# Kernel tuning notes

Measured on AMD Instinct MI355X. Metric: run time of the kernel, lower is better.

## Reference

```python
import jax, jax.numpy as jnp
import numpy as np

MUL = 32
HEAD_DIM = 16
CLIP = 5.0
EPS = 1e-6
INV_SQRTD = 1.0 / np.sqrt(HEAD_DIM)
ENV_BLOCKS = (1, 3)          # 0e, 1o
TP_BLOCKS = (1, 1, 3, 3)     # 0e(0x0), 0e(1x1), 1o(0x1), 1o(1x0)


def so3_layernorm(x, g, block_dims):
    """x: [..., MUL, D]; per-irrep-block RMS norm over (mul, components), affine scale g [MUL, n_blocks]."""
    out, i = [], 0
    for b, d in enumerate(block_dims):
        blk = x[..., i:i + d]
        n = jnp.sqrt(jnp.mean(blk * blk, axis=(-2, -1), keepdims=True) + EPS)
        out.append(blk / n * g[:, b][:, None])
        i += d
    return jnp.concatenate(out, axis=-1)


def scatter_softmax(logits, seg, num_segments):
    """softmax over edges grouped by destination node. logits [E, M]."""
    m = jax.ops.segment_max(logits, seg, num_segments=num_segments)
    e = jnp.exp(logits - m[seg])
    d = jax.ops.segment_sum(e, seg, num_segments=num_segments)
    return e / d[seg]


def setup_inputs() -> dict:
    key = jax.random.key(0)
    ks = jax.random.split(key, 16)
    N, E, LAT, NODE_DIM, COND, HID = 16384, 262144, 64, 64, 32, 128
    sc = lambda f: f ** -0.5
    return {
        "node_attrs": jax.random.normal(ks[0], (N, NODE_DIM), jnp.float32),
        "scalar_state": jax.random.normal(ks[1], (E, LAT), jnp.float32),
        "equiv_state": jax.random.normal(ks[2], (E, MUL, 4), jnp.float32),
        "edge_conditioning": jax.random.normal(ks[3], (E, COND), jnp.float32),
        "residual_update_coeff": jax.random.uniform(ks[4], (1,), jnp.float32),
        "W_env1": jax.random.normal(ks[5], (LAT + COND, HID), jnp.float32) * sc(LAT + COND),
        "b_env1": jnp.zeros((HID,), jnp.float32),
        "W_env2": jax.random.normal(ks[6], (HID, MUL * 2), jnp.float32) * sc(HID),
        "Wq": jax.random.normal(ks[7], (NODE_DIM, MUL * HEAD_DIM), jnp.float32) * sc(NODE_DIM),
        "Wk": jax.random.normal(ks[8], (LAT, MUL * HEAD_DIM), jnp.float32) * sc(LAT),
        "g_env": jnp.ones((MUL, 2), jnp.float32),
        "g_tp": jnp.ones((MUL, 4), jnp.float32),
        "Wp1": jax.random.normal(ks[9], (MUL * 2 + COND, HID), jnp.float32) * sc(MUL * 2 + COND),
        "bp1": jnp.zeros((HID,), jnp.float32),
        "Wp2": jax.random.normal(ks[10], (HID, LAT + MUL * 4), jnp.float32) * sc(HID),
        "edge_src": jax.random.randint(ks[11], (E,), 0, N),
    }


def reference(node_attrs, scalar_state, equiv_state, edge_conditioning,
              residual_update_coeff, W_env1, b_env1, W_env2, Wq, Wk,
              g_env, g_tp, Wp1, bp1, Wp2, edge_src):
    N = node_attrs.shape[0]
    E = scalar_state.shape[0]
    LAT = scalar_state.shape[1]

    # --- env_embed_mlp: scalar MLP -> per-(mul, irrep-block) gates on equiv state ---
    x = jnp.concatenate([scalar_state, edge_conditioning], axis=-1)
    h = jax.nn.silu(x @ W_env1 + b_env1)
    w = (h @ W_env2).reshape(E, MUL, 2)                    # [E, mul, 2 blocks]
    w_exp = jnp.repeat(w, np.array(ENV_BLOCKS), axis=-1, total_repeat_length=4)
    env_edges = equiv_state * w_exp                        # [E, mul, 4]

    # --- attention: edge-gathered query, clipped logits, scatter softmax ---
    Q = (node_attrs[edge_src] @ Wq).reshape(E, MUL, HEAD_DIM)
    K = (scalar_state @ Wk).reshape(E, MUL, HEAD_DIM)
    logits = jnp.einsum('emd,emd->em', Q, K) * INV_SQRTD
    logits = jnp.clip(logits, -CLIP, CLIP)
    attn = scatter_softmax(logits, edge_src, N)            # [E, mul]
    env_edges = env_edges * attn[..., None]

    # --- scatter-sum to nodes, SO3 layernorm, gather back ---
    env_nodes = jax.ops.segment_sum(env_edges, edge_src, num_segments=N)  # [N, mul, 4]
    env_nodes = so3_layernorm(env_nodes, g_env, ENV_BLOCKS)
    edge_local_env = env_nodes[edge_src]                   # [E, mul, 4]

    # --- Contracter, uuu mode, instructions: 0x0->0, 1x1->0, 0x1->1, 1x0->1 ---
    s1, v1 = equiv_state[..., 0], equiv_state[..., 1:4]
    s2, v2 = edge_local_env[..., 0], edge_local_env[..., 1:4]
    o0a = s1 * s2                                          # 0e
    o0b = jnp.einsum('emi,emi->em', v1, v2) / np.sqrt(3.0) # 0e (CG of 1x1->0)
    o1a = s1[..., None] * v2                               # 1o
    o1b = v1 * s2[..., None]                               # 1o
    tp_out = jnp.concatenate([o0a[..., None], o0b[..., None], o1a, o1b], axis=-1)  # [E, mul, 8]
    tp_out = so3_layernorm(tp_out, g_tp, TP_BLOCKS)

    # --- projection: scalar MLP -> new scalar latent + per-path weights mixing equiv blocks ---
    scalars = tp_out[..., :2].reshape(E, MUL * 2)
    xp = jnp.concatenate([scalars, edge_conditioning], axis=-1)
    hp = jax.nn.silu(xp @ Wp1 + bp1)
    op = hp @ Wp2
    new_scalar = op[:, :LAT]
    pw = op[:, LAT:].reshape(E, MUL, 4)
    new_s = pw[..., 0] * tp_out[..., 0] + pw[..., 1] * tp_out[..., 1]
    new_v = pw[..., 2:3] * tp_out[..., 2:5] + pw[..., 3:4] * tp_out[..., 5:8]
    new_equiv = jnp.concatenate([new_s[..., None], new_v], axis=-1)  # [E, mul, 4]

    # --- residual streams ---
    c_old = jax.lax.rsqrt(residual_update_coeff ** 2 + 1.0)
    c_new = residual_update_coeff * c_old
    scalar_out = c_old * scalar_state + c_new * new_scalar
    equiv_out = c_old * equiv_state + c_new * new_equiv
    return scalar_out, equiv_out
```

## Files before the change

kernel.cpp:

```cpp
#include <hip/hip_runtime.h>
#include <math.h>

#define EPSF 1e-6f
#define ST1 68
#define ST2 36

__device__ __forceinline__ float silu_f(float x){ return x * (1.0f/(1.0f + __expf(-x))); }

__global__ __launch_bounds__(256) void k_qnode(
    const float* __restrict__ na, const float* __restrict__ Wq,
    float* __restrict__ qn)
{
  __shared__ float At[64*16];
  const int nb = blockIdx.x * 16;
  const int t = threadIdx.x;
  for (int f = t; f < 16*64; f += 256){ int n = f>>6, i = f&63; At[i*16+n] = na[(size_t)(nb+n)*64 + i]; }
  __syncthreads();
  float acc0[16], acc1[16];
#pragma unroll
  for (int n=0;n<16;n++){ acc0[n]=0.f; acc1[n]=0.f; }
  for (int i=0;i<64;i++){
    float w0 = Wq[(size_t)i*512 + t];
    float w1 = Wq[(size_t)i*512 + t + 256];
#pragma unroll
    for (int n=0;n<16;n++){ float a = At[i*16+n]; acc0[n] = fmaf(a,w0,acc0[n]); acc1[n] = fmaf(a,w1,acc1[n]); }
  }
#pragma unroll
  for (int n=0;n<16;n++){
    qn[(size_t)(nb+n)*512 + t]       = acc0[n];
    qn[(size_t)(nb+n)*512 + t + 256] = acc1[n];
  }
}

__global__ __launch_bounds__(256) void k_edge1(
    const float* __restrict__ ssi, const float* __restrict__ cond,
    const float* __restrict__ equiv, const int* __restrict__ esrc,
    const float* __restrict__ W1, const float* __restrict__ b1,
    const float* __restrict__ W2, const float* __restrict__ Wk,
    const float* __restrict__ qn,
    float* __restrict__ denom, float* __restrict__ num)
{
  __shared__ float sm[96*ST1 + 128*ST1];
  __shared__ int src_l[64];
  float* Xt = sm;
  float* Ht = sm + 96*ST1;
  float* wl = Ht;
  float* lg = Ht + 64*ST1;
  const int e0 = blockIdx.x * 64;
  const int t = threadIdx.x;
  const int r0 = (t>>5)*8;

  for (int f=t; f<64*64; f+=256){ int r=f>>6, i=f&63; Xt[i*ST1+r] = ssi[(size_t)(e0+r)*64 + i]; }
  for (int f=t; f<64*32; f+=256){ int r=f>>5, i=f&31; Xt[(64+i)*ST1+r] = cond[(size_t)(e0+r)*32 + i]; }
  if (t < 64) src_l[t] = esrc[e0+t];
  __syncthreads();

  {
    const int c0 = (t&31)*4;
    float acc[8][4];
#pragma unroll
    for (int rr=0;rr<8;rr++){ acc[rr][0]=0;acc[rr][1]=0;acc[rr][2]=0;acc[rr][3]=0; }
    for (int i=0;i<96;i++){
      const float4 w  = *(const float4*)(W1 + (size_t)i*128 + c0);
      const float4 xa = *(const float4*)(Xt + i*ST1 + r0);
      const float4 xb = *(const float4*)(Xt + i*ST1 + r0 + 4);
      const float xv[8] = {xa.x,xa.y,xa.z,xa.w,xb.x,xb.y,xb.z,xb.w};
#pragma unroll
      for (int rr=0;rr<8;rr++){
        acc[rr][0] = fmaf(xv[rr], w.x, acc[rr][0]);
        acc[rr][1] = fmaf(xv[rr], w.y, acc[rr][1]);
        acc[rr][2] = fmaf(xv[rr], w.z, acc[rr][2]);
        acc[rr][3] = fmaf(xv[rr], w.w, acc[rr][3]);
      }
    }
    const float4 bb = *(const float4*)(b1 + c0);
    const float bv[4] = {bb.x,bb.y,bb.z,bb.w};
#pragma unroll
    for (int cc=0;cc<4;cc++)
#pragma unroll
      for (int rr=0;rr<8;rr++)
        Ht[(c0+cc)*ST1 + r0+rr] = silu_f(acc[rr][cc] + bv[cc]);
  }
  __syncthreads();

  float wacc[8][2];
  {
    const int c0 = (t&31)*2;
#pragma unroll
    for (int rr=0;rr<8;rr++){ wacc[rr][0]=0; wacc[rr][1]=0; }
    for (int j=0;j<128;j++){
      const float2 w  = *(const float2*)(W2 + (size_t)j*64 + c0);
      const float4 ha = *(const float4*)(Ht + j*ST1 + r0);
      const float4 hb = *(const float4*)(Ht + j*ST1 + r0 + 4);
      const float hv[8] = {ha.x,ha.y,ha.z,ha.w,hb.x,hb.y,hb.z,hb.w};
#pragma unroll
      for (int rr=0;rr<8;rr++){
        wacc[rr][0] = fmaf(hv[rr], w.x, wacc[rr][0]);
        wacc[rr][1] = fmaf(hv[rr], w.y, wacc[rr][1]);
      }
    }
  }
  __syncthreads();
  {
    const int c0 = (t&31)*2;
#pragma unroll
    for (int cc=0;cc<2;cc++)
#pragma unroll
      for (int rr=0;rr<8;rr++)
        wl[(c0+cc)*ST1 + r0+rr] = wacc[rr][cc];
  }
  __syncthreads();

  for (int it=0; it<4; it++){
    const int c0 = (t&31)*4 + it*128;
    float acc[8][4];
#pragma unroll
    for (int rr=0;rr<8;rr++){ acc[rr][0]=0;acc[rr][1]=0;acc[rr][2]=0;acc[rr][3]=0; }
    for (int i=0;i<64;i++){
      const float4 w  = *(const float4*)(Wk + (size_t)i*512 + c0);
      const float4 xa = *(const float4*)(Xt + i*ST1 + r0);
      const float4 xb = *(const float4*)(Xt + i*ST1 + r0 + 4);
      const float xv[8] = {xa.x,xa.y,xa.z,xa.w,xb.x,xb.y,xb.z,xb.w};
#pragma unroll
      for (int rr=0;rr<8;rr++){
        acc[rr][0] = fmaf(xv[rr], w.x, acc[rr][0]);
        acc[rr][1] = fmaf(xv[rr], w.y, acc[rr][1]);
        acc[rr][2] = fmaf(xv[rr], w.z, acc[rr][2]);
        acc[rr][3] = fmaf(xv[rr], w.w, acc[rr][3]);
      }
    }
    const int m = c0 >> 4;
#pragma unroll
    for (int rr=0;rr<8;rr++){
      const float4 q = *(const float4*)(qn + (size_t)src_l[r0+rr]*512 + c0);
      float p = acc[rr][0]*q.x + acc[rr][1]*q.y + acc[rr][2]*q.z + acc[rr][3]*q.w;
      p += __shfl_xor(p, 1);
      p += __shfl_xor(p, 2);
      if ((t&3)==0) lg[(r0+rr)*32 + m] = p;
    }
  }
  __syncthreads();

  for (int f=t; f<64*32; f+=256){
    int r=f>>5, m=f&31;
    float l = lg[f] * 0.25f;
    l = fminf(5.0f, fmaxf(-5.0f, l));
    float el = __expf(l);
    lg[f] = el;
    atomicAdd(denom + (size_t)src_l[r]*32 + m, el);
  }
  __syncthreads();

  for (int f=t; f<64*128; f+=256){
    int r=f>>7, mc=f&127, m=mc>>2, c=mc&3;
    float el = lg[r*32+m];
    float wv = wl[(m*2 + (c?1:0))*ST1 + r];
    float ev = equiv[(size_t)(e0+r)*128 + mc];
    atomicAdd(num + (size_t)src_l[r]*128 + mc, el*wv*ev);
  }
}

__global__ __launch_bounds__(128) void k_dnorm(
    float* __restrict__ num, const float* __restrict__ denom,
    const float* __restrict__ g_env)
{
  __shared__ float red[128];
  __shared__ float inv0s, inv1s;
  const int n = blockIdx.x, t = threadIdx.x;
  const int m = t>>2, c = t&3;
  const float d = denom[(size_t)n*32+m];
  const float x = (d > 0.0f) ? num[(size_t)n*128+t]/d : 0.0f;
  red[t] = x*x;
  __syncthreads();
  if (t < 32){
    float p0 = red[4*t];
    float p1 = red[4*t+1]+red[4*t+2]+red[4*t+3];
#pragma unroll
    for (int k=1;k<32;k<<=1){ p0 += __shfl_xor(p0,k); p1 += __shfl_xor(p1,k); }
    if (t==0){ inv0s = 1.0f/sqrtf(p0*(1.0f/32.0f) + EPSF); inv1s = 1.0f/sqrtf(p1*(1.0f/96.0f) + EPSF); }
  }
  __syncthreads();
  const float g = g_env[m*2 + (c?1:0)];
  num[(size_t)n*128+t] = x * (c ? inv1s : inv0s) * g;
}

__global__ __launch_bounds__(256) void k_edge2(
    const float* __restrict__ ssi, const float* __restrict__ cond,
    const float* __restrict__ equiv, const int* __restrict__ esrc,
    const float* __restrict__ envn, const float* __restrict__ g_tp,
    const float* __restrict__ Wp1, const float* __restrict__ bp1,
    const float* __restrict__ Wp2, const float* __restrict__ ruc,
    float* __restrict__ outs, float* __restrict__ oute)
{
  __shared__ float envl[32*128];
  __shared__ float Xp[96*ST2];
  __shared__ float Hp[128*ST2];
  __shared__ float inv_l[32*4];
  __shared__ int src_l[32];
  const int e0 = blockIdx.x * 32;
  const int t = threadIdx.x;
  if (t < 32) src_l[t] = esrc[e0+t];
  __syncthreads();
  for (int f=t; f<32*128; f+=256){ int r=f>>7, cx=f&127; envl[f] = envn[(size_t)src_l[r]*128 + cx]; }
  for (int f=t; f<32*32; f+=256){ int r=f>>5, i=f&31; Xp[(64+i)*ST2 + r] = cond[(size_t)(e0+r)*32 + i]; }
  __syncthreads();

  {
    const int r = t>>3, sub = t&7;
    float ss0=0,ss1=0,ss2=0,ss3=0;
#pragma unroll
    for (int mm=0;mm<4;mm++){
      const int m = sub*4+mm;
      const float4 e4 = *(const float4*)(equiv + (size_t)(e0+r)*128 + 4*m);
      const float4 n4 = *(const float4*)(envl + r*128 + 4*m);
      const float tp0 = e4.x*n4.x;
      const float dv  = e4.y*n4.y + e4.z*n4.z + e4.w*n4.w;
      const float tp1 = dv*0.5773502691896258f;
      ss0 += tp0*tp0;
      ss1 += tp1*tp1;
      ss2 += e4.x*e4.x*(n4.y*n4.y + n4.z*n4.z + n4.w*n4.w);
      ss3 += n4.x*n4.x*(e4.y*e4.y + e4.z*e4.z + e4.w*e4.w);
    }
#pragma unroll
    for (int k=1;k<8;k<<=1){
      ss0 += __shfl_xor(ss0,k); ss1 += __shfl_xor(ss1,k);
      ss2 += __shfl_xor(ss2,k); ss3 += __shfl_xor(ss3,k);
    }
    if (sub == 0){
      inv_l[r*4+0] = 1.0f/sqrtf(ss0*(1.0f/32.0f) + EPSF);
      inv_l[r*4+1] = 1.0f/sqrtf(ss1*(1.0f/32.0f) + EPSF);
      inv_l[r*4+2] = 1.0f/sqrtf(ss2*(1.0f/96.0f) + EPSF);
      inv_l[r*4+3] = 1.0f/sqrtf(ss3*(1.0f/96.0f) + EPSF);
    }
  }
  __syncthreads();

  for (int f=t; f<32*64; f+=256){
    const int r = f>>6, col = f&63, m = col>>1;
    const float4 e4 = *(const float4*)(equiv + (size_t)(e0+r)*128 + 4*m);
    const float4 n4 = *(const float4*)(envl + r*128 + 4*m);
    float v;
    if (col & 1)
      v = (e4.y*n4.y + e4.z*n4.z + e4.w*n4.w)*0.5773502691896258f * inv_l[r*4+1] * g_tp[m*4+1];
    else
      v = e4.x*n4.x * inv_l[r*4+0] * g_tp[m*4+0];
    Xp[col*ST2 + r] = v;
  }
  __syncthreads();

  const int r0 = (t>>5)*4;
  {
    const int c0 = (t&31)*4;
    float acc[4][4];
#pragma unroll
    for (int rr=0;rr<4;rr++){acc[rr][0]=0;acc[rr][1]=0;acc[rr][2]=0;acc[rr][3]=0;}
    for (int i=0;i<96;i++){
      const float4 w  = *(const float4*)(Wp1 + (size_t)i*128 + c0);
      const float4 xa = *(const float4*)(Xp + i*ST2 + r0);
      const float xv[4] = {xa.x,xa.y,xa.z,xa.w};
#pragma unroll
      for (int rr=0;rr<4;rr++){
        acc[rr][0]=fmaf(xv[rr],w.x,acc[rr][0]);
        acc[rr][1]=fmaf(xv[rr],w.y,acc[rr][1]);
        acc[rr][2]=fmaf(xv[rr],w.z,acc[rr][2]);
        acc[rr][3]=fmaf(xv[rr],w.w,acc[rr][3]);
      }
    }
    const float4 bb = *(const float4*)(bp1 + c0);
    const float bv[4] = {bb.x,bb.y,bb.z,bb.w};
#pragma unroll
    for (int cc=0;cc<4;cc++)
#pragma unroll
      for (int rr=0;rr<4;rr++)
        Hp[(c0+cc)*ST2 + r0+rr] = silu_f(acc[rr][cc] + bv[cc]);
  }
  __syncthreads();

  const float rv = ruc[0];
  const float c_old = 1.0f/sqrtf(rv*rv + 1.0f);
  const float c_new = rv * c_old;

  {
    const int c0 = (t&31)*2;
    float acc[4][2];
#pragma unroll
    for (int rr=0;rr<4;rr++){acc[rr][0]=0;acc[rr][1]=0;}
    for (int j=0;j<128;j++){
      const float2 w  = *(const float2*)(Wp2 + (size_t)j*192 + c0);
      const float4 ha = *(const float4*)(Hp + j*ST2 + r0);
      const float hv[4] = {ha.x,ha.y,ha.z,ha.w};
#pragma unroll
      for (int rr=0;rr<4;rr++){
        acc[rr][0]=fmaf(hv[rr],w.x,acc[rr][0]);
        acc[rr][1]=fmaf(hv[rr],w.y,acc[rr][1]);
      }
    }
#pragma unroll
    for (int rr=0;rr<4;rr++){
      const size_t e = (size_t)(e0+r0+rr);
#pragma unroll
      for (int cc=0;cc<2;cc++)
        outs[e*64 + c0+cc] = c_old*ssi[e*64 + c0+cc] + c_new*acc[rr][cc];
    }
  }

  {
    const int m = t&31;
    float acc[4][4];
#pragma unroll
    for (int rr=0;rr<4;rr++){acc[rr][0]=0;acc[rr][1]=0;acc[rr][2]=0;acc[rr][3]=0;}
    for (int j=0;j<128;j++){
      const float4 w  = *(const float4*)(Wp2 + (size_t)j*192 + 64 + 4*m);
      const float4 ha = *(const float4*)(Hp + j*ST2 + r0);
      const float hv[4] = {ha.x,ha.y,ha.z,ha.w};
#pragma unroll
      for (int rr=0;rr<4;rr++){
        acc[rr][0]=fmaf(hv[rr],w.x,acc[rr][0]);
        acc[rr][1]=fmaf(hv[rr],w.y,acc[rr][1]);
        acc[rr][2]=fmaf(hv[rr],w.z,acc[rr][2]);
        acc[rr][3]=fmaf(hv[rr],w.w,acc[rr][3]);
      }
    }
    const float g2 = g_tp[m*4+2], g3 = g_tp[m*4+3];
#pragma unroll
    for (int rr=0;rr<4;rr++){
      const int r = r0+rr;
      const size_t e = (size_t)(e0+r);
      const float4 e4 = *(const float4*)(equiv + e*128 + 4*m);
      const float4 n4 = *(const float4*)(envl + r*128 + 4*m);
      const float tpn0 = Xp[(2*m)*ST2 + r];
      const float tpn1 = Xp[(2*m+1)*ST2 + r];
      const float a2 = acc[rr][2]*inv_l[r*4+2]*g2;
      const float a3 = acc[rr][3]*inv_l[r*4+3]*g3;
      float4 o;
      o.x = c_old*e4.x + c_new*(acc[rr][0]*tpn0 + acc[rr][1]*tpn1);
      o.y = c_old*e4.y + c_new*(a2*(e4.x*n4.y) + a3*(e4.y*n4.x));
      o.z = c_old*e4.z + c_new*(a2*(e4.x*n4.z) + a3*(e4.z*n4.x));
      o.w = c_old*e4.w + c_new*(a2*(e4.x*n4.w) + a3*(e4.w*n4.x));
      *(float4*)(oute + e*128 + 4*m) = o;
    }
  }
}

extern "C" void kernel_launch(void* const* d_in, const int* in_sizes, int n_in,
                              void* d_out, int out_size, void* d_ws, size_t ws_size,
                              hipStream_t stream)
{
  const float* na   = (const float*)d_in[0];
  const float* ssi  = (const float*)d_in[1];
  const float* eqv  = (const float*)d_in[2];
  const float* cond = (const float*)d_in[3];
  const float* ruc  = (const float*)d_in[4];
  const float* W1   = (const float*)d_in[5];
  const float* b1   = (const float*)d_in[6];
  const float* W2   = (const float*)d_in[7];
  const float* Wq   = (const float*)d_in[8];
  const float* Wk   = (const float*)d_in[9];
  const float* ge   = (const float*)d_in[10];
  const float* gt   = (const float*)d_in[11];
  const float* Wp1  = (const float*)d_in[12];
  const float* bp1  = (const float*)d_in[13];
  const float* Wp2  = (const float*)d_in[14];
  const int*   esrc = (const int*)d_in[15];

  const int N = in_sizes[0] / 64;
  const int E = in_sizes[1] / 64;

  float* denom = (float*)d_ws;
  float* num   = denom + (size_t)N*32;
  float* qn    = num   + (size_t)N*128;
  float* outs  = (float*)d_out;
  float* oute  = outs + (size_t)E*64;

  hipMemsetAsync(d_ws, 0, (size_t)N*160*sizeof(float), stream);
  k_qnode<<<N/16, 256, 0, stream>>>(na, Wq, qn);
  k_edge1<<<E/64, 256, 0, stream>>>(ssi, cond, eqv, esrc, W1, b1, W2, Wk, qn, denom, num);
  k_dnorm<<<N, 128, 0, stream>>>(num, denom, ge);
  k_edge2<<<E/32, 256, 0, stream>>>(ssi, cond, eqv, esrc, num, gt, Wp1, bp1, Wp2, ruc, outs, oute);
}
```

Baseline: 1.502 ms.

## Restructure edge kernels to row-major smem tiles, 32-edge blocks, k-unrolled GEMMs

Switches the shared-memory staging in both edge kernels from transposed (feature-major) to row-major (edge-major) layouts with padded strides. This allows float4 global loads, and the GEMM inner loops are unrolled by 4 along K with vectorized smem reads. k_edge1 now processes 32 edges per block instead of 64, halving register tiles and smem, and adds occupancy hints via launch_bounds. The scatter loop now issues four atomics per float4 of equiv. The intent is fewer, wider memory ops and higher occupancy, at the cost of twice as many edge1 blocks and repeated weight reads.

```diff
diff --git a/kernel.cpp b/kernel.cpp
--- a/kernel.cpp
+++ b/kernel.cpp
@@ -2,8 +2,8 @@
 #include <math.h>
 
 #define EPSF 1e-6f
-#define ST1 68
-#define ST2 36
+#define STX 100
+#define STH 132
 
 __device__ __forceinline__ float silu_f(float x){ return x * (1.0f/(1.0f + __expf(-x))); }
 
@@ -32,7 +32,7 @@
   }
 }
 
-__global__ __launch_bounds__(256) void k_edge1(
+__global__ __launch_bounds__(256,4) void k_edge1(
     const float* __restrict__ ssi, const float* __restrict__ cond,
     const float* __restrict__ equiv, const int* __restrict__ esrc,
     const float* __restrict__ W1, const float* __restrict__ b1,
@@ -40,99 +40,107 @@
     const float* __restrict__ qn,
     float* __restrict__ denom, float* __restrict__ num)
 {
-  __shared__ float sm[96*ST1 + 128*ST1];
-  __shared__ int src_l[64];
-  float* Xt = sm;
-  float* Ht = sm + 96*ST1;
-  float* wl = Ht;
-  float* lg = Ht + 64*ST1;
-  const int e0 = blockIdx.x * 64;
+  __shared__ float Xs[32*STX];
+  __shared__ float Hs[32*STH];
+  __shared__ float lg[32*32];
+  __shared__ int src_l[32];
+  const int e0 = blockIdx.x * 32;
   const int t = threadIdx.x;
-  const int r0 = (t>>5)*8;
-
-  for (int f=t; f<64*64; f+=256){ int r=f>>6, i=f&63; Xt[i*ST1+r] = ssi[(size_t)(e0+r)*64 + i]; }
-  for (int f=t; f<64*32; f+=256){ int r=f>>5, i=f&31; Xt[(64+i)*ST1+r] = cond[(size_t)(e0+r)*32 + i]; }
-  if (t < 64) src_l[t] = esrc[e0+t];
+  const int r0 = (t>>5)*4;
+
+  if (t < 32) src_l[t] = esrc[e0+t];
+  for (int f=t; f<512; f+=256){ int r=f>>4, q=(f&15)*4;
+    *(float4*)(Xs + r*STX + q) = *(const float4*)(ssi + (size_t)(e0+r)*64 + q); }
+  { int f=t; int r=f>>3, q=(f&7)*4;
+    *(float4*)(Xs + r*STX + 64 + q) = *(const float4*)(cond + (size_t)(e0+r)*32 + q); }
   __syncthreads();
 
   {
     const int c0 = (t&31)*4;
-    float acc[8][4];
-#pragma unroll
-    for (int rr=0;rr<8;rr++){ acc[rr][0]=0;acc[rr][1]=0;acc[rr][2]=0;acc[rr][3]=0; }
-    for (int i=0;i<96;i++){
-      const float4 w  = *(const float4*)(W1 + (size_t)i*128 + c0);
-      const float4 xa = *(const float4*)(Xt + i*ST1 + r0);
-      const float4 xb = *(const float4*)(Xt + i*ST1 + r0 + 4);
-      const float xv[8] = {xa.x,xa.y,xa.z,xa.w,xb.x,xb.y,xb.z,xb.w};
-#pragma unroll
-      for (int rr=0;rr<8;rr++){
-        acc[rr][0] = fmaf(xv[rr], w.x, acc[rr][0]);
-        acc[rr][1] = fmaf(xv[rr], w.y, acc[rr][1]);
-        acc[rr][2] = fmaf(xv[rr], w.z, acc[rr][2]);
-        acc[rr][3] = fmaf(xv[rr], w.w, acc[rr][3]);
+    float acc[4][4] = {};
+    for (int i0=0;i0<96;i0+=4){
+      float4 wv[4], xv[4];
+#pragma unroll
+      for (int k=0;k<4;k++) wv[k] = *(const float4*)(W1 + (size_t)(i0+k)*128 + c0);
+#pragma unroll
+      for (int rr=0;rr<4;rr++) xv[rr] = *(const float4*)(Xs + (r0+rr)*STX + i0);
+#pragma unroll
+      for (int rr=0;rr<4;rr++){
+        const float xs[4] = {xv[rr].x,xv[rr].y,xv[rr].z,xv[rr].w};
+#pragma unroll
+        for (int k=0;k<4;k++){
+          acc[rr][0] = fmaf(xs[k], wv[k].x, acc[rr][0]);
+          acc[rr][1] = fmaf(xs[k], wv[k].y, acc[rr][1]);
+          acc[rr][2] = fmaf(xs[k], wv[k].z, acc[rr][2]);
+          acc[rr][3] = fmaf(xs[k], wv[k].w, acc[rr][3]);
+        }
       }
     }
     const float4 bb = *(const float4*)(b1 + c0);
-    const float bv[4] = {bb.x,bb.y,bb.z,bb.w};
-#pragma unroll
-    for (int cc=0;cc<4;cc++)
-#pragma unroll
-      for (int rr=0;rr<8;rr++)
-        Ht[(c0+cc)*ST1 + r0+rr] = silu_f(acc[rr][cc] + bv[cc]);
-  }
-  __syncthreads();
-
-  float wacc[8][2];
+#pragma unroll
+    for (int rr=0;rr<4;rr++){
+      float4 h;
+      h.x = silu_f(acc[rr][0]+bb.x); h.y = silu_f(acc[rr][1]+bb.y);
+      h.z = silu_f(acc[rr][2]+bb.z); h.w = silu_f(acc[rr][3]+bb.w);
+      *(float4*)(Hs + (r0+rr)*STH + c0) = h;
+    }
+  }
+  __syncthreads();
+
+  float wacc[4][2] = {};
   {
     const int c0 = (t&31)*2;
-#pragma unroll
-    for (int rr=0;rr<8;rr++){ wacc[rr][0]=0; wacc[rr][1]=0; }
-    for (int j=0;j<128;j++){
-      const float2 w  = *(const float2*)(W2 + (size_t)j*64 + c0);
-      const float4 ha = *(const float4*)(Ht + j*ST1 + r0);
-      const float4 hb = *(const float4*)(Ht + j*ST1 + r0 + 4);
-      const float hv[8] = {ha.x,ha.y,ha.z,ha.w,hb.x,hb.y,hb.z,hb.w};
-#pragma unroll
-      for (int rr=0;rr<8;rr++){
-        wacc[rr][0] = fmaf(hv[rr], w.x, wacc[rr][0]);
-        wacc[rr][1] = fmaf(hv[rr], w.y, wacc[rr][1]);
-      }
-    }
-  }
-  __syncthreads();
+    for (int j0=0;j0<128;j0+=4){
+      float2 w2[4]; float4 hv[4];
+#pragma unroll
+      for (int k=0;k<4;k++) w2[k] = *(const float2*)(W2 + (size_t)(j0+k)*64 + c0);
+#pragma unroll
+      for (int rr=0;rr<4;rr++) hv[rr] = *(const float4*)(Hs + (r0+rr)*STH + j0);
+#pragma unroll
+      for (int rr=0;rr<4;rr++){
+        const float hs[4] = {hv[rr].x,hv[rr].y,hv[rr].z,hv[rr].w};
+#pragma unroll
+        for (int k=0;k<4;k++){
+          wacc[rr][0] = fmaf(hs[k], w2[k].x, wacc[rr][0]);
+          wacc[rr][1] = fmaf(hs[k], w2[k].y, wacc[rr][1]);
+        }
+      }
+    }
+  }
+  __syncthreads();
+  float* wl = Hs;
   {
     const int c0 = (t&31)*2;
 #pragma unroll
-    for (int cc=0;cc<2;cc++)
-#pragma unroll
-      for (int rr=0;rr<8;rr++)
-        wl[(c0+cc)*ST1 + r0+rr] = wacc[rr][cc];
-  }
-  __syncthreads();
+    for (int rr=0;rr<4;rr++)
+      *(float2*)(wl + (r0+rr)*66 + c0) = make_float2(wacc[rr][0], wacc[rr][1]);
+  }
 
   for (int it=0; it<4; it++){
-    const int c0 = (t&31)*4 + it*128;
-    float acc[8][4];
-#pragma unroll
-    for (int rr=0;rr<8;rr++){ acc[rr][0]=0;acc[rr][1]=0;acc[rr][2]=0;acc[rr][3]=0; }
-    for (int i=0;i<64;i++){
-      const float4 w  = *(const float4*)(Wk + (size_t)i*512 + c0);
-      const float4 xa = *(const float4*)(Xt + i*ST1 + r0);
-      const float4 xb = *(const float4*)(Xt + i*ST1 + r0 + 4);
-      const float xv[8] = {xa.x,xa.y,xa.z,xa.w,xb.x,xb.y,xb.z,xb.w};
-#pragma unroll
-      for (int rr=0;rr<8;rr++){
-        acc[rr][0] = fmaf(xv[rr], w.x, acc[rr][0]);
-        acc[rr][1] = fmaf(xv[rr], w.y, acc[rr][1]);
-        acc[rr][2] = fmaf(xv[rr], w.z, acc[rr][2]);
-        acc[rr][3] = fmaf(xv[rr], w.w, acc[rr][3]);
-      }
-    }
-    const int m = c0 >> 4;
-#pragma unroll
-    for (int rr=0;rr<8;rr++){
-      const float4 q = *(const float4*)(qn + (size_t)src_l[r0+rr]*512 + c0);
+    const int c0k = (t&31)*4 + it*128;
+    float acc[4][4] = {};
+    for (int i0=0;i0<64;i0+=4){
+      float4 wv[4], xv[4];
+#pragma unroll
+      for (int k=0;k<4;k++) wv[k] = *(const float4*)(Wk + (size_t)(i0+k)*512 + c0k);
+#pragma unroll
+      for (int rr=0;rr<4;rr++) xv[rr] = *(const float4*)(Xs + (r0+rr)*STX + i0);
+#pragma unroll
+      for (int rr=0;rr<4;rr++){
+        const float xs[4] = {xv[rr].x,xv[rr].y,xv[rr].z,xv[rr].w};
+#pragma unroll
+        for (int k=0;k<4;k++){
+          acc[rr][0] = fmaf(xs[k], wv[k].x, acc[rr][0]);
+          acc[rr][1] = fmaf(xs[k], wv[k].y, acc[rr][1]);
+          acc[rr][2] = fmaf(xs[k], wv[k].z, acc[rr][2]);
+          acc[rr][3] = fmaf(xs[k], wv[k].w, acc[rr][3]);
+        }
+      }
+    }
+    const int m = ((t&31)>>2) + it*8;
+#pragma unroll
+    for (int rr=0;rr<4;rr++){
+      const float4 q = *(const float4*)(qn + (size_t)src_l[r0+rr]*512 + c0k);
       float p = acc[rr][0]*q.x + acc[rr][1]*q.y + acc[rr][2]*q.z + acc[rr][3]*q.w;
       p += __shfl_xor(p, 1);
       p += __shfl_xor(p, 2);
@@ -141,7 +149,7 @@
   }
   __syncthreads();
 
-  for (int f=t; f<64*32; f+=256){
+  for (int f=t; f<1024; f+=256){
     int r=f>>5, m=f&31;
     float l = lg[f] * 0.25f;
     l = fminf(5.0f, fmaxf(-5.0f, l));
@@ -151,12 +159,17 @@
   }
   __syncthreads();
 
-  for (int f=t; f<64*128; f+=256){
-    int r=f>>7, mc=f&127, m=mc>>2, c=mc&3;
-    float el = lg[r*32+m];
-    float wv = wl[(m*2 + (c?1:0))*ST1 + r];
-    float ev = equiv[(size_t)(e0+r)*128 + mc];
-    atomicAdd(num + (size_t)src_l[r]*128 + mc, el*wv*ev);
+  for (int f=t; f<1024; f+=256){
+    int r=f>>5, m=f&31;
+    const float el = lg[r*32+m];
+    const float w0 = wl[r*66 + 2*m]   * el;
+    const float w1 = wl[r*66 + 2*m+1] * el;
+    const float4 ev = *(const float4*)(equiv + ((size_t)(e0+r)*32 + m)*4);
+    float* np = num + (size_t)src_l[r]*128 + 4*m;
+    atomicAdd(np+0, w0*ev.x);
+    atomicAdd(np+1, w1*ev.y);
+    atomicAdd(np+2, w1*ev.z);
+    atomicAdd(np+3, w1*ev.w);
   }
 }
 
@@ -184,7 +197,7 @@
   num[(size_t)n*128+t] = x * (c ? inv1s : inv0s) * g;
 }
 
-__global__ __launch_bounds__(256) void k_edge2(
+__global__ __launch_bounds__(256,3) void k_edge2(
     const float* __restrict__ ssi, const float* __restrict__ cond,
     const float* __restrict__ equiv, const int* __restrict__ esrc,
     const float* __restrict__ envn, const float* __restrict__ g_tp,
@@ -192,17 +205,20 @@
     const float* __restrict__ Wp2, const float* __restrict__ ruc,
     float* __restrict__ outs, float* __restrict__ oute)
 {
-  __shared__ float envl[32*128];
-  __shared__ float Xp[96*ST2];
-  __shared__ float Hp[128*ST2];
+  __shared__ float envl[32*STH];
+  __shared__ float Xp[32*STX];
+  __shared__ float Hp[32*STH];
   __shared__ float inv_l[32*4];
   __shared__ int src_l[32];
   const int e0 = blockIdx.x * 32;
   const int t = threadIdx.x;
+  const int r0 = (t>>5)*4;
   if (t < 32) src_l[t] = esrc[e0+t];
   __syncthreads();
-  for (int f=t; f<32*128; f+=256){ int r=f>>7, cx=f&127; envl[f] = envn[(size_t)src_l[r]*128 + cx]; }
-  for (int f=t; f<32*32; f+=256){ int r=f>>5, i=f&31; Xp[(64+i)*ST2 + r] = cond[(size_t)(e0+r)*32 + i]; }
+  for (int f=t; f<1024; f+=256){ int r=f>>5, q=(f&31)*4;
+    *(float4*)(envl + r*STH + q) = *(const float4*)(envn + (size_t)src_l[r]*128 + q); }
+  { int f=t; int r=f>>3, q=(f&7)*4;
+    *(float4*)(Xp + r*STX + 64 + q) = *(const float4*)(cond + (size_t)(e0+r)*32 + q); }
   __syncthreads();
 
   {
@@ -211,8 +227,8 @@
 #pragma unroll
     for (int mm=0;mm<4;mm++){
       const int m = sub*4+mm;
-      const float4 e4 = *(const float4*)(equiv + (size_t)(e0+r)*128 + 4*m);
-      const float4 n4 = *(const float4*)(envl + r*128 + 4*m);
+      const float4 e4 = *(const float4*)(equiv + ((size_t)(e0+r)*32 + m)*4);
+      const float4 n4 = *(const float4*)(envl + r*STH + 4*m);
       const float tp0 = e4.x*n4.x;
       const float dv  = e4.y*n4.y + e4.z*n4.z + e4.w*n4.w;
       const float tp1 = dv*0.5773502691896258f;
@@ -235,44 +251,48 @@
   }
   __syncthreads();
 
-  for (int f=t; f<32*64; f+=256){
+  for (int f=t; f<2048; f+=256){
     const int r = f>>6, col = f&63, m = col>>1;
-    const float4 e4 = *(const float4*)(equiv + (size_t)(e0+r)*128 + 4*m);
-    const float4 n4 = *(const float4*)(envl + r*128 + 4*m);
+    const float4 e4 = *(const float4*)(equiv + ((size_t)(e0+r)*32 + m)*4);
+    const float4 n4 = *(const float4*)(envl + r*STH + 4*m);
     float v;
     if (col & 1)
       v = (e4.y*n4.y + e4.z*n4.z + e4.w*n4.w)*0.5773502691896258f * inv_l[r*4+1] * g_tp[m*4+1];
     else
       v = e4.x*n4.x * inv_l[r*4+0] * g_tp[m*4+0];
-    Xp[col*ST2 + r] = v;
-  }
-  __syncthreads();
-
-  const int r0 = (t>>5)*4;
+    Xp[r*STX + col] = v;
+  }
+  __syncthreads();
+
   {
     const int c0 = (t&31)*4;
-    float acc[4][4];
-#pragma unroll
-    for (int rr=0;rr<4;rr++){acc[rr][0]=0;acc[rr][1]=0;acc[rr][2]=0;acc[rr][3]=0;}
-    for (int i=0;i<96;i++){
-      const float4 w  = *(const float4*)(Wp1 + (size_t)i*128 + c0);
-      const float4 xa = *(const float4*)(Xp + i*ST2 + r0);
-      const float xv[4] = {xa.x,xa.y,xa.z,xa.w};
-#pragma unroll
-      for (int rr=0;rr<4;rr++){
-        acc[rr][0]=fmaf(xv[rr],w.x,acc[rr][0]);
-        acc[rr][1]=fmaf(xv[rr],w.y,acc[rr][1]);
-        acc[rr][2]=fmaf(xv[rr],w.z,acc[rr][2]);
-        acc[rr][3]=fmaf(xv[rr],w.w,acc[rr][3]);
+    float acc[4][4] = {};
+    for (int i0=0;i0<96;i0+=4){
+      float4 wv[4], xv[4];
+#pragma unroll
+      for (int k=0;k<4;k++) wv[k] = *(const float4*)(Wp1 + (size_t)(i0+k)*128 + c0);
+#pragma unroll
+      for (int rr=0;rr<4;rr++) xv[rr] = *(const float4*)(Xp + (r0+rr)*STX + i0);
+#pragma unroll
+      for (int rr=0;rr<4;rr++){
+        const float xs[4] = {xv[rr].x,xv[rr].y,xv[rr].z,xv[rr].w};
+#pragma unroll
+        for (int k=0;k<4;k++){
+          acc[rr][0] = fmaf(xs[k], wv[k].x, acc[rr][0]);
+          acc[rr][1] = fmaf(xs[k], wv[k].y, acc[rr][1]);
+          acc[rr][2] = fmaf(xs[k], wv[k].z, acc[rr][2]);
+          acc[rr][3] = fmaf(xs[k], wv[k].w, acc[rr][3]);
+        }
       }
     }
     const float4 bb = *(const float4*)(bp1 + c0);
-    const float bv[4] = {bb.x,bb.y,bb.z,bb.w};
-#pragma unroll
-    for (int cc=0;cc<4;cc++)
-#pragma unroll
-      for (int rr=0;rr<4;rr++)
-        Hp[(c0+cc)*ST2 + r0+rr] = silu_f(acc[rr][cc] + bv[cc]);
+#pragma unroll
+    for (int rr=0;rr<4;rr++){
+      float4 h;
+      h.x = silu_f(acc[rr][0]+bb.x); h.y = silu_f(acc[rr][1]+bb.y);
+      h.z = silu_f(acc[rr][2]+bb.z); h.w = silu_f(acc[rr][3]+bb.w);
+      *(float4*)(Hp + (r0+rr)*STH + c0) = h;
+    }
   }
   __syncthreads();
 
@@ -282,43 +302,51 @@
 
   {
     const int c0 = (t&31)*2;
-    float acc[4][2];
-#pragma unroll
-    for (int rr=0;rr<4;rr++){acc[rr][0]=0;acc[rr][1]=0;}
-    for (int j=0;j<128;j++){
-      const float2 w  = *(const float2*)(Wp2 + (size_t)j*192 + c0);
-      const float4 ha = *(const float4*)(Hp + j*ST2 + r0);
-      const float hv[4] = {ha.x,ha.y,ha.z,ha.w};
-#pragma unroll
-      for (int rr=0;rr<4;rr++){
-        acc[rr][0]=fmaf(hv[rr],w.x,acc[rr][0]);
-        acc[rr][1]=fmaf(hv[rr],w.y,acc[rr][1]);
+    float acc[4][2] = {};
+    for (int j0=0;j0<128;j0+=4){
+      float2 w2[4]; float4 hv[4];
+#pragma unroll
+      for (int k=0;k<4;k++) w2[k] = *(const float2*)(Wp2 + (size_t)(j0+k)*192 + c0);
+#pragma unroll
+      for (int rr=0;rr<4;rr++) hv[rr] = *(const float4*)(Hp + (r0+rr)*STH + j0);
+#pragma unroll
+      for (int rr=0;rr<4;rr++){
+        const float hs[4] = {hv[rr].x,hv[rr].y,hv[rr].z,hv[rr].w};
+#pragma unroll
+        for (int k=0;k<4;k++){
+          acc[rr][0] = fmaf(hs[k], w2[k].x, acc[rr][0]);
+          acc[rr][1] = fmaf(hs[k], w2[k].y, acc[rr][1]);
+        }
       }
     }
 #pragma unroll
     for (int rr=0;rr<4;rr++){
       const size_t e = (size_t)(e0+r0+rr);
-#pragma unroll
-      for (int cc=0;cc<2;cc++)
-        outs[e*64 + c0+cc] = c_old*ssi[e*64 + c0+cc] + c_new*acc[rr][cc];
+      const float2 s2 = *(const float2*)(ssi + e*64 + c0);
+      float2 o2; o2.x = c_old*s2.x + c_new*acc[rr][0]; o2.y = c_old*s2.y + c_new*acc[rr][1];
+      *(float2*)(outs + e*64 + c0) = o2;
     }
   }
 
   {
     const int m = t&31;
-    float acc[4][4];
-#pragma unroll
-    for (int rr=0;rr<4;rr++){acc[rr][0]=0;acc[rr][1]=0;acc[rr][2]=0;acc[rr][3]=0;}
-    for (int j=0;j<128;j++){
-      const float4 w  = *(const float4*)(Wp2 + (size_t)j*192 + 64 + 4*m);
-      const float4 ha = *(const float4*)(Hp + j*ST2 + r0);
-      const float hv[4] = {ha.x,ha.y,ha.z,ha.w};
-#pragma unroll
-      for (int rr=0;rr<4;rr++){
-        acc[rr][0]=fmaf(hv[rr],w.x,acc[rr][0]);
-        acc[rr][1]=fmaf(hv[rr],w.y,acc[rr][1]);
-        acc[rr][2]=fmaf(hv[rr],w.z,acc[rr][2]);
-        acc[rr][3]=fmaf(hv[rr],w.w,acc[rr][3]);
+    float acc[4][4] = {};
+    for (int j0=0;j0<128;j0+=4){
+      float4 w4[4]; float4 hv[4];
+#pragma unroll
+      for (int k=0;k<4;k++) w4[k] = *(const float4*)(Wp2 + (size_t)(j0+k)*192 + 64 + 4*m);
+#pragma unroll
+      for (int rr=0;rr<4;rr++) hv[rr] = *(const float4*)(Hp + (r0+rr)*STH + j0);
+#pragma unroll
+      for (int rr=0;rr<4;rr++){
+        const float hs[4] = {hv[rr].x,hv[rr].y,hv[rr].z,hv[rr].w};
+#pragma unroll
+        for (int k=0;k<4;k++){
+          acc[rr][0] = fmaf(hs[k], w4[k].x, acc[rr][0]);
+          acc[rr][1] = fmaf(hs[k], w4[k].y, acc[rr][1]);
+          acc[rr][2] = fmaf(hs[k], w4[k].z, acc[rr][2]);
+          acc[rr][3] = fmaf(hs[k], w4[k].w, acc[rr][3]);
+        }
       }
     }
     const float g2 = g_tp[m*4+2], g3 = g_tp[m*4+3];
@@ -326,10 +354,10 @@
     for (int rr=0;rr<4;rr++){
       const int r = r0+rr;
       const size_t e = (size_t)(e0+r);
-      const float4 e4 = *(const float4*)(equiv + e*128 + 4*m);
-      const float4 n4 = *(const float4*)(envl + r*128 + 4*m);
-      const float tpn0 = Xp[(2*m)*ST2 + r];
-      const float tpn1 = Xp[(2*m+1)*ST2 + r];
+      const float4 e4 = *(const float4*)(equiv + (e*32 + m)*4);
+      const float4 n4 = *(const float4*)(envl + r*STH + 4*m);
+      const float tpn0 = Xp[r*STX + 2*m];
+      const float tpn1 = Xp[r*STX + 2*m+1];
       const float a2 = acc[rr][2]*inv_l[r*4+2]*g2;
       const float a3 = acc[rr][3]*inv_l[r*4+3]*g3;
       float4 o;
@@ -374,7 +402,7 @@
 
   hipMemsetAsync(d_ws, 0, (size_t)N*160*sizeof(float), stream);
   k_qnode<<<N/16, 256, 0, stream>>>(na, Wq, qn);
-  k_edge1<<<E/64, 256, 0, stream>>>(ssi, cond, eqv, esrc, W1, b1, W2, Wk, qn, denom, num);
+  k_edge1<<<E/32, 256, 0, stream>>>(ssi, cond, eqv, esrc, W1, b1, W2, Wk, qn, denom, num);
   k_dnorm<<<N, 128, 0, stream>>>(num, denom, ge);
   k_edge2<<<E/32, 256, 0, stream>>>(ssi, cond, eqv, esrc, num, gt, Wp1, bp1, Wp2, ruc, outs, oute);
 }
```

After: 1.399 ms. 6.9% less time.
